# Kernel tuning notes

Hardware: AMD Instinct MI355X
Metric: run time of the kernel (lower is better)

Reference implementation:

```python
import jax, jax.numpy as jnp
import numpy as np

D_MODEL = 1280
NUM_HEADS = 16
GROUPS = 5
D_K = D_MODEL // NUM_HEADS  # 80
B, S = 4, 1024


def setup_inputs() -> dict:
    key = jax.random.key(0)
    ks = jax.random.split(key, 12)
    lim_dk = 1.0 / np.sqrt(D_K)
    lim_dm = 1.0 / np.sqrt(D_MODEL)
    return {
        "src": jax.random.normal(ks[0], (B, S, D_MODEL), jnp.float32),
        "k": jax.random.normal(ks[1], (B, S, D_MODEL), jnp.float32),
        "v": jax.random.normal(ks[2], (B, S, D_MODEL), jnp.float32),
        # per-head Linear(d_k, d_k) stacked: weight [H, d_k(out), d_k(in)], bias [H, d_k]
        "Wq": jax.random.uniform(ks[3], (NUM_HEADS, D_K, D_K), jnp.float32, -lim_dk, lim_dk),
        "bq": jax.random.uniform(ks[4], (NUM_HEADS, D_K), jnp.float32, -lim_dk, lim_dk),
        "Wk": jax.random.uniform(ks[5], (NUM_HEADS, D_K, D_K), jnp.float32, -lim_dk, lim_dk),
        "bk": jax.random.uniform(ks[6], (NUM_HEADS, D_K), jnp.float32, -lim_dk, lim_dk),
        "Wv": jax.random.uniform(ks[7], (NUM_HEADS, D_K, D_K), jnp.float32, -lim_dk, lim_dk),
        "bv": jax.random.uniform(ks[8], (NUM_HEADS, D_K), jnp.float32, -lim_dk, lim_dk),
        # output Linear(d_model, d_model)
        "Wo": jax.random.uniform(ks[9], (D_MODEL, D_MODEL), jnp.float32, -lim_dm, lim_dm),
        "bo": jax.random.uniform(ks[10], (D_MODEL,), jnp.float32, -lim_dm, lim_dm),
    }


def reference(src, k, v, Wq, bq, Wk, bk, Wv, bv, Wo, bo):
    # NOTE: original module ignores k, v args; q/k/v all derived from src.
    b, s, d = src.shape
    cpg = d // GROUPS
    # channel shuffle: [B,S,G,C] -> [B,S,C,G] -> [B,S,D]
    x = src.reshape(b, s, GROUPS, cpg).swapaxes(-1, -2).reshape(b, s, d)
    # split heads: [B, H, S, d_k]
    xh = x.reshape(b, s, NUM_HEADS, D_K).transpose(0, 2, 1, 3)
    # per-head distinct linears, batched over heads (torch Linear: x @ W.T + b)
    q = jnp.einsum("bhsd,hed->bhse", xh, Wq) + bq[None, :, None, :]
    kk = jnp.einsum("bhsd,hed->bhse", xh, Wk) + bk[None, :, None, :]
    vv = jnp.einsum("bhsd,hed->bhse", xh, Wv) + bv[None, :, None, :]
    scores = jnp.einsum("bhqd,bhkd->bhqk", q, kk) / jnp.sqrt(jnp.float32(D_K))
    p = jax.nn.softmax(scores, axis=-1)
    heads = jnp.einsum("bhqk,bhkd->bhqd", p, vv)
    concat = heads.transpose(0, 2, 1, 3).reshape(b, s, d)
    return concat @ Wo.T + bo
```

## Files before the change

kernel.cpp:

```cpp
#include <hip/hip_runtime.h>
#include <hip/hip_bf16.h>

#define D_MODEL 1280
#define NUM_HEADS 16
#define D_K 80
#define DP 96
#define SEQ 1024
#define BATCH 4
#define BH (BATCH*NUM_HEADS)

typedef __hip_bfloat16 bf16;
typedef short short8 __attribute__((ext_vector_type(8)));
typedef short short4v __attribute__((ext_vector_type(4)));
typedef float f32x4 __attribute__((ext_vector_type(4)));

__device__ __forceinline__ float b2f(bf16 x) { return __bfloat162float(x); }
__device__ __forceinline__ bf16 f2b(float x) { return __float2bfloat16(x); }
__device__ __forceinline__ short bbits(float x) {
    union { bf16 b; short s; } u; u.b = __float2bfloat16(x); return u.s;
}

#define MFMA16(a, b, c) __builtin_amdgcn_mfma_f32_16x16x32_bf16(a, b, c, 0, 0, 0)

__global__ __launch_bounds__(256) void cvtw_kernel(
    const float* __restrict__ Wq, const float* __restrict__ Wk,
    const float* __restrict__ Wv, bf16* __restrict__ Wcat)
{
    int idx = blockIdx.x * 256 + threadIdx.x;
    int col = idx % 96;
    int row = (idx / 96) % 240;
    int h   = idx / (96 * 240);
    int mat = row / 80, e = row % 80;
    const float* W = (mat == 0) ? Wq : (mat == 1) ? Wk : Wv;
    float v = (col < 80) ? W[(size_t)(h * 80 + e) * 80 + col] : 0.f;
    Wcat[idx] = f2b(v);
}

__global__ __launch_bounds__(256) void cvt_kernel(
    const float* __restrict__ Wo, bf16* __restrict__ Wb)
{
    int idx = (blockIdx.x * 256 + threadIdx.x) * 4;
    float4 v = *(const float4*)(Wo + idx);
    Wb[idx]     = f2b(v.x);
    Wb[idx + 1] = f2b(v.y);
    Wb[idx + 2] = f2b(v.z);
    Wb[idx + 3] = f2b(v.w);
}

__global__ __launch_bounds__(256) void qkv_kernel(
    const float* __restrict__ src,
    const float* __restrict__ bq, const float* __restrict__ bk,
    const float* __restrict__ bv, const bf16* __restrict__ Wcat,
    bf16* __restrict__ Qb, bf16* __restrict__ Kb, bf16* __restrict__ Vg)
{
    __shared__ bf16 Xs[128 * 104];
    const int h = blockIdx.y;
    const int b = blockIdx.x >> 3;
    const int s0 = (blockIdx.x & 7) * 128;
    const int tid = threadIdx.x;
    const int wave = tid >> 6, lane = tid & 63;
    const int lquad = lane >> 4, lcol = lane & 15;
    const int bh = b * NUM_HEADS + h;

    #pragma unroll
    for (int it = 0; it < 10; it++) {
        int idx = tid + it * 256;
        int i = idx / 20, rem = idx % 20, c = rem >> 2, q4 = rem & 3;
        float4 v = *(const float4*)(src + (size_t)(b * SEQ + s0 + i) * D_MODEL
                                    + c * 256 + h * 16 + q4 * 4);
        bf16* x = Xs + i * 104 + c;
        x[(q4 * 4 + 0) * 5] = f2b(v.x);
        x[(q4 * 4 + 1) * 5] = f2b(v.y);
        x[(q4 * 4 + 2) * 5] = f2b(v.z);
        x[(q4 * 4 + 3) * 5] = f2b(v.w);
    }
    {
        int i = tid >> 1, half = tid & 1;
        *(uint4*)(Xs + i * 104 + 80 + half * 8) = make_uint4(0, 0, 0, 0);
    }
    __syncthreads();

    short8 xf[2][3];
    #pragma unroll
    for (int mt = 0; mt < 2; mt++)
        #pragma unroll
        for (int ks = 0; ks < 3; ks++)
            xf[mt][ks] = *(const short8*)(Xs + (wave*32 + mt*16 + lcol)*104 + ks*32 + lquad*8);

    const bf16* Wh = Wcat + (size_t)h * 240 * 96;
    const float qscale = 1.4426950408889634f * 0.11180339887498949f;

    #pragma unroll
    for (int mat = 0; mat < 2; mat++) {
        const bf16* Wm = Wh + mat * 80 * 96;
        short8 wf[5][3];
        #pragma unroll
        for (int n = 0; n < 5; n++)
            #pragma unroll
            for (int ks = 0; ks < 3; ks++)
                wf[n][ks] = *(const short8*)(Wm + (n*16 + lcol)*96 + ks*32 + lquad*8);

        f32x4 acc[2][5];
        #pragma unroll
        for (int mt = 0; mt < 2; mt++)
            #pragma unroll
            for (int n = 0; n < 5; n++)
                #pragma unroll
                for (int r = 0; r < 4; r++) acc[mt][n][r] = 0.f;

        #pragma unroll
        for (int ks = 0; ks < 3; ks++)
            #pragma unroll
            for (int n = 0; n < 5; n++) {
                acc[0][n] = MFMA16(xf[0][ks], wf[n][ks], acc[0][n]);
                acc[1][n] = MFMA16(xf[1][ks], wf[n][ks], acc[1][n]);
            }

        const float* bias = (mat == 0) ? bq : bk;
        bf16* Out = (mat == 0) ? Qb : Kb;
        const float scale = (mat == 0) ? qscale : 1.f;
        #pragma unroll
        for (int n = 0; n < 5; n++) {
            float bb = bias[h * 80 + n * 16 + lcol];
            #pragma unroll
            for (int mt = 0; mt < 2; mt++)
                #pragma unroll
                for (int r = 0; r < 4; r++) {
                    int srow = s0 + wave*32 + mt*16 + lquad*4 + r;
                    Out[((size_t)bh * SEQ + srow) * DP + n*16 + lcol] =
                        f2b((acc[mt][n][r] + bb) * scale);
                }
        }
    }
    {
        int i = tid >> 1, half = tid & 1;
        size_t row = ((size_t)bh * SEQ + s0 + i) * DP + 80 + half * 8;
        *(uint4*)(Qb + row) = make_uint4(0, 0, 0, 0);
        *(uint4*)(Kb + row) = make_uint4(0, 0, 0, 0);
    }

    {
        const bf16* Wm = Wh + 2 * 80 * 96;
        short8 wf[5][3];
        #pragma unroll
        for (int m = 0; m < 5; m++)
            #pragma unroll
            for (int ks = 0; ks < 3; ks++)
                wf[m][ks] = *(const short8*)(Wm + (m*16 + lcol)*96 + ks*32 + lquad*8);

        f32x4 acc[5][2];
        #pragma unroll
        for (int m = 0; m < 5; m++)
            #pragma unroll
            for (int nt = 0; nt < 2; nt++)
                #pragma unroll
                for (int r = 0; r < 4; r++) acc[m][nt][r] = 0.f;

        #pragma unroll
        for (int ks = 0; ks < 3; ks++)
            #pragma unroll
            for (int m = 0; m < 5; m++) {
                acc[m][0] = MFMA16(wf[m][ks], xf[0][ks], acc[m][0]);
                acc[m][1] = MFMA16(wf[m][ks], xf[1][ks], acc[m][1]);
            }

        #pragma unroll
        for (int m = 0; m < 5; m++) {
            float4 bb4 = *(const float4*)(bv + h * 80 + m * 16 + lquad * 4);
            float bb[4] = {bb4.x, bb4.y, bb4.z, bb4.w};
            #pragma unroll
            for (int nt = 0; nt < 2; nt++)
                #pragma unroll
                for (int r = 0; r < 4; r++) {
                    int e = m*16 + lquad*4 + r;
                    int token = s0 + wave*32 + nt*16 + lcol;
                    Vg[((size_t)bh * D_K + e) * SEQ + token] =
                        f2b(acc[m][nt][r] + bb[r]);
                }
        }
    }
}

__global__ __launch_bounds__(128) void attn_kernel(
    const bf16* __restrict__ Qb, const bf16* __restrict__ Kb,
    const bf16* __restrict__ Vg, bf16* __restrict__ Cc)
{
    __shared__ char smem[38144];
    bf16* Qs = (bf16*)smem;
    bf16* Ks = (bf16*)(smem + 13312);
    bf16* Vt = (bf16*)(smem + 26624);

    const int tid = threadIdx.x;
    const int wave = tid >> 6, lane = tid & 63;
    const int lquad = lane >> 4, lcol = lane & 15;
    const int bh = blockIdx.x;
    const int b = bh >> 4, h = bh & 15;
    const int q0 = blockIdx.y * 64;

    {
        const uint4* qg = (const uint4*)(Qb + ((size_t)bh * SEQ + q0) * DP);
        #pragma unroll
        for (int i = 0; i < 6; i++) {
            int idx = tid + i * 128, r = idx / 12, c = idx % 12;
            *(uint4*)(Qs + r * 104 + c * 8) = qg[idx];
        }
    }
    __syncthreads();

    short8 qf[2][3];
    #pragma unroll
    for (int nt = 0; nt < 2; nt++)
        #pragma unroll
        for (int ks = 0; ks < 3; ks++)
            qf[nt][ks] = *(const short8*)(Qs + (wave*32 + nt*16 + lcol)*104 + ks*32 + lquad*8);

    f32x4 Oacc[2][5];
    #pragma unroll
    for (int mt = 0; mt < 2; mt++)
        #pragma unroll
        for (int ne = 0; ne < 5; ne++)
            #pragma unroll
            for (int r = 0; r < 4; r++) Oacc[mt][ne][r] = 0.f;

    float lsum[2] = {0.f, 0.f};
    bf16* Pw = (bf16*)(smem + wave * 4608);

    for (int kt = 0; kt < 16; kt++) {
        __syncthreads();
        {
            const uint4* kg = (const uint4*)(Kb + ((size_t)bh * SEQ + kt * 64) * DP);
            #pragma unroll
            for (int i = 0; i < 6; i++) {
                int idx = tid + i * 128, r = idx / 12, c = idx % 12;
                *(uint4*)(Ks + r * 104 + c * 8) = kg[idx];
            }
        }
        #pragma unroll
        for (int i = 0; i < 5; i++) {
            int idx = tid + i * 128;
            int e = idx >> 3, c = idx & 7;
            *(uint4*)(Vt + e * 72 + c * 8) =
                *(const uint4*)(Vg + ((size_t)bh * D_K + e) * SEQ + kt * 64 + c * 8);
        }
        __syncthreads();

        f32x4 st[4][2];
        #pragma unroll
        for (int mt = 0; mt < 4; mt++)
            #pragma unroll
            for (int nt = 0; nt < 2; nt++)
                #pragma unroll
                for (int r = 0; r < 4; r++) st[mt][nt][r] = 0.f;

        #pragma unroll
        for (int ks = 0; ks < 3; ks++) {
            #pragma unroll
            for (int mt = 0; mt < 4; mt++) {
                short8 af = *(const short8*)(Ks + (mt*16 + lcol)*104 + ks*32 + lquad*8);
                st[mt][0] = MFMA16(af, qf[0][ks], st[mt][0]);
                st[mt][1] = MFMA16(af, qf[1][ks], st[mt][1]);
            }
        }

        #pragma unroll
        for (int nt = 0; nt < 2; nt++) {
            #pragma unroll
            for (int mt = 0; mt < 4; mt++) {
                short4v pk;
                #pragma unroll
                for (int r = 0; r < 4; r++) {
                    float p = __builtin_amdgcn_exp2f(st[mt][nt][r]);
                    lsum[nt] += p;
                    pk[r] = bbits(p);
                }
                *(short4v*)(Pw + (nt*16 + lcol)*72 + mt*16 + lquad*4) = pk;
            }
        }

        #pragma unroll
        for (int js = 0; js < 2; js++) {
            short8 pf[2];
            #pragma unroll
            for (int mt = 0; mt < 2; mt++)
                pf[mt] = *(const short8*)(Pw + (mt*16 + lcol)*72 + js*32 + lquad*8);
            #pragma unroll
            for (int ne = 0; ne < 5; ne++) {
                short8 vf = *(const short8*)(Vt + (ne*16 + lcol)*72 + js*32 + lquad*8);
                Oacc[0][ne] = MFMA16(pf[0], vf, Oacc[0][ne]);
                Oacc[1][ne] = MFMA16(pf[1], vf, Oacc[1][ne]);
            }
        }
    }

    float inv[2];
    #pragma unroll
    for (int nt = 0; nt < 2; nt++) {
        float s = lsum[nt];
        s += __shfl_xor(s, 16);
        s += __shfl_xor(s, 32);
        inv[nt] = 1.f / s;
    }
    #pragma unroll
    for (int mt = 0; mt < 2; mt++) {
        f32x4 li;
        #pragma unroll
        for (int r = 0; r < 4; r++)
            li[r] = __shfl(inv[mt], (lane & 48) | (lquad*4 + r));
        #pragma unroll
        for (int ne = 0; ne < 5; ne++)
            #pragma unroll
            for (int r = 0; r < 4; r++) {
                int s_row = q0 + wave*32 + mt*16 + lquad*4 + r;
                int e = ne*16 + lcol;
                Cc[(size_t)(b * SEQ + s_row) * D_MODEL + h * D_K + e] =
                    f2b(Oacc[mt][ne][r] * li[r]);
            }
    }
}

__global__ __launch_bounds__(256) void proj_kernel(
    const bf16* __restrict__ Cc, const bf16* __restrict__ Wb,
    const float* __restrict__ bo, float* __restrict__ out)
{
    __shared__ bf16 As[128 * 72];
    __shared__ bf16 Bs[128 * 72];
    const int tid = threadIdx.x;
    const int wave = tid >> 6, lane = tid & 63;
    const int lquad = lane >> 4, lcol = lane & 15;
    const int t0 = blockIdx.x * 128, o0 = blockIdx.y * 128;
    const int mrow = (wave & 1) * 64, ncol = (wave >> 1) * 64;

    f32x4 acc[4][4];
    #pragma unroll
    for (int mt = 0; mt < 4; mt++)
        #pragma unroll
        for (int nt = 0; nt < 4; nt++)
            #pragma unroll
            for (int r = 0; r < 4; r++) acc[mt][nt][r] = 0.f;

    for (int kc = 0; kc < 20; kc++) {
        __syncthreads();
        #pragma unroll
        for (int i = 0; i < 4; i++) {
            int idx = tid + i * 256;
            int r = idx >> 3, c = idx & 7;
            *(uint4*)(As + r * 72 + c * 8) =
                *(const uint4*)(Cc + (size_t)(t0 + r) * D_MODEL + kc * 64 + c * 8);
            *(uint4*)(Bs + r * 72 + c * 8) =
                *(const uint4*)(Wb + (size_t)(o0 + r) * D_MODEL + kc * 64 + c * 8);
        }
        __syncthreads();
        #pragma unroll
        for (int ks = 0; ks < 2; ks++) {
            short8 am[4], bn[4];
            #pragma unroll
            for (int t = 0; t < 4; t++) {
                am[t] = *(const short8*)(As + (mrow + t*16 + lcol)*72 + ks*32 + lquad*8);
                bn[t] = *(const short8*)(Bs + (ncol + t*16 + lcol)*72 + ks*32 + lquad*8);
            }
            #pragma unroll
            for (int mt = 0; mt < 4; mt++)
                #pragma unroll
                for (int nt = 0; nt < 4; nt++)
                    acc[mt][nt] = MFMA16(am[mt], bn[nt], acc[mt][nt]);
        }
    }

    #pragma unroll
    for (int nt = 0; nt < 4; nt++) {
        float bias = bo[o0 + ncol + nt*16 + lcol];
        #pragma unroll
        for (int mt = 0; mt < 4; mt++)
            #pragma unroll
            for (int r = 0; r < 4; r++)
                out[(size_t)(t0 + mrow + mt*16 + lquad*4 + r) * D_MODEL
                    + o0 + ncol + nt*16 + lcol] = acc[mt][nt][r] + bias;
    }
}

extern "C" void kernel_launch(void* const* d_in, const int* in_sizes, int n_in,
                              void* d_out, int out_size, void* d_ws, size_t ws_size,
                              hipStream_t stream) {
    const float* src = (const float*)d_in[0];
    const float* Wq = (const float*)d_in[3];
    const float* bq = (const float*)d_in[4];
    const float* Wk = (const float*)d_in[5];
    const float* bk = (const float*)d_in[6];
    const float* Wv = (const float*)d_in[7];
    const float* bv = (const float*)d_in[8];
    const float* Wo = (const float*)d_in[9];
    const float* bo = (const float*)d_in[10];
    float* out = (float*)d_out;

    char* ws = (char*)d_ws;
    bf16* Qb = (bf16*)(ws);
    bf16* Kb = (bf16*)(ws + (size_t)12582912);
    bf16* Vg = (bf16*)(ws + (size_t)25165824);
    bf16* Cc = (bf16*)(ws + (size_t)35651584);
    bf16* Wcat = (bf16*)(ws + (size_t)35651584);
    bf16* Wb = (bf16*)(ws + (size_t)46137344);

    cvtw_kernel<<<dim3(1440), 256, 0, stream>>>(Wq, Wk, Wv, Wcat);
    cvt_kernel<<<dim3(D_MODEL * D_MODEL / 1024), 256, 0, stream>>>(Wo, Wb);
    qkv_kernel<<<dim3(BATCH * SEQ / 128, NUM_HEADS), 256, 0, stream>>>(
        src, bq, bk, bv, Wcat, Qb, Kb, Vg);
    attn_kernel<<<dim3(BH, SEQ / 64), 128, 0, stream>>>(Qb, Kb, Vg, Cc);
    proj_kernel<<<dim3(SEQ * BATCH / 128, D_MODEL / 128), 256, 0, stream>>>(
        Cc, Wb, bo, out);
}
```

Measured before the change: 197.0 us.

## Double-buffer K tiles, read V directly to registers, merge weight conversion kernels

Reworks the attention kernel to use 256-thread blocks covering 128 queries, keep Q fragments in registers loaded straight from global memory, and double-buffer K tiles in shared memory with register prefetch. This cuts the barriers per iteration from two to one. V fragments are read directly from global into registers instead of being staged through LDS, and s_setprio is raised around the MFMA sections. The two weight-conversion kernels are merged into one launch to remove a launch. The trade-off is more register pressure and uncoalesced per-lane V loads from global memory.

```diff
diff --git a/kernel.cpp b/kernel.cpp
--- a/kernel.cpp
+++ b/kernel.cpp
@@ -22,29 +22,28 @@
 
 #define MFMA16(a, b, c) __builtin_amdgcn_mfma_f32_16x16x32_bf16(a, b, c, 0, 0, 0)
 
-__global__ __launch_bounds__(256) void cvtw_kernel(
+__global__ __launch_bounds__(256) void cvt_all_kernel(
     const float* __restrict__ Wq, const float* __restrict__ Wk,
-    const float* __restrict__ Wv, bf16* __restrict__ Wcat)
-{
-    int idx = blockIdx.x * 256 + threadIdx.x;
-    int col = idx % 96;
-    int row = (idx / 96) % 240;
-    int h   = idx / (96 * 240);
-    int mat = row / 80, e = row % 80;
-    const float* W = (mat == 0) ? Wq : (mat == 1) ? Wk : Wv;
-    float v = (col < 80) ? W[(size_t)(h * 80 + e) * 80 + col] : 0.f;
-    Wcat[idx] = f2b(v);
-}
-
-__global__ __launch_bounds__(256) void cvt_kernel(
+    const float* __restrict__ Wv, bf16* __restrict__ Wcat,
     const float* __restrict__ Wo, bf16* __restrict__ Wb)
 {
-    int idx = (blockIdx.x * 256 + threadIdx.x) * 4;
-    float4 v = *(const float4*)(Wo + idx);
-    Wb[idx]     = f2b(v.x);
-    Wb[idx + 1] = f2b(v.y);
-    Wb[idx + 2] = f2b(v.z);
-    Wb[idx + 3] = f2b(v.w);
+    if (blockIdx.x < 1440) {
+        int idx = blockIdx.x * 256 + threadIdx.x;
+        int col = idx % 96;
+        int row = (idx / 96) % 240;
+        int h   = idx / (96 * 240);
+        int mat = row / 80, e = row % 80;
+        const float* W = (mat == 0) ? Wq : (mat == 1) ? Wk : Wv;
+        float v = (col < 80) ? W[(size_t)(h * 80 + e) * 80 + col] : 0.f;
+        Wcat[idx] = f2b(v);
+    } else {
+        int idx = ((blockIdx.x - 1440) * 256 + threadIdx.x) * 4;
+        float4 v = *(const float4*)(Wo + idx);
+        Wb[idx]     = f2b(v.x);
+        Wb[idx + 1] = f2b(v.y);
+        Wb[idx + 2] = f2b(v.z);
+        Wb[idx + 3] = f2b(v.w);
+    }
 }
 
 __global__ __launch_bounds__(256) void qkv_kernel(
@@ -181,121 +180,143 @@
     }
 }
 
-__global__ __launch_bounds__(128) void attn_kernel(
+__global__ __launch_bounds__(256, 2) void attn_kernel(
     const bf16* __restrict__ Qb, const bf16* __restrict__ Kb,
     const bf16* __restrict__ Vg, bf16* __restrict__ Cc)
 {
-    __shared__ char smem[38144];
-    bf16* Qs = (bf16*)smem;
-    bf16* Ks = (bf16*)(smem + 13312);
-    bf16* Vt = (bf16*)(smem + 26624);
-
+    __shared__ char smem[45056];
     const int tid = threadIdx.x;
     const int wave = tid >> 6, lane = tid & 63;
     const int lquad = lane >> 4, lcol = lane & 15;
     const int bh = blockIdx.x;
     const int b = bh >> 4, h = bh & 15;
-    const int q0 = blockIdx.y * 64;
-
+    const int q0 = blockIdx.y * 128;
+
+    int koff[3];
+    #pragma unroll
+    for (int i = 0; i < 3; i++) {
+        int idx = tid + i * 256;
+        koff[i] = (idx / 12) * 104 + (idx % 12) * 8;
+    }
+
+    short8 qf[2][3];
+    #pragma unroll
+    for (int nt = 0; nt < 2; nt++)
+        #pragma unroll
+        for (int ks = 0; ks < 3; ks++)
+            qf[nt][ks] = *(const short8*)(
+                Qb + ((size_t)bh * SEQ + q0 + wave*32 + nt*16 + lcol) * DP
+                   + ks*32 + lquad*8);
+
+    uint4 kr[3];
     {
-        const uint4* qg = (const uint4*)(Qb + ((size_t)bh * SEQ + q0) * DP);
-        #pragma unroll
-        for (int i = 0; i < 6; i++) {
-            int idx = tid + i * 128, r = idx / 12, c = idx % 12;
-            *(uint4*)(Qs + r * 104 + c * 8) = qg[idx];
-        }
+        const uint4* kg = (const uint4*)(Kb + (size_t)bh * SEQ * DP);
+        #pragma unroll
+        for (int i = 0; i < 3; i++) kr[i] = kg[tid + i * 256];
+    }
+    {
+        bf16* Ks0 = (bf16*)(smem + 18432);
+        #pragma unroll
+        for (int i = 0; i < 3; i++) *(uint4*)(Ks0 + koff[i]) = kr[i];
     }
     __syncthreads();
 
-    short8 qf[2][3];
+    const bf16* Vrow[5];
+    #pragma unroll
+    for (int ne = 0; ne < 5; ne++)
+        Vrow[ne] = Vg + ((size_t)bh * D_K + ne*16 + lcol) * SEQ + lquad*8;
+
+    f32x4 Oacc[2][5];
+    #pragma unroll
+    for (int mt = 0; mt < 2; mt++)
+        #pragma unroll
+        for (int ne = 0; ne < 5; ne++)
+            #pragma unroll
+            for (int r = 0; r < 4; r++) Oacc[mt][ne][r] = 0.f;
+
+    f32x4 lsum4[2];
     #pragma unroll
     for (int nt = 0; nt < 2; nt++)
         #pragma unroll
-        for (int ks = 0; ks < 3; ks++)
-            qf[nt][ks] = *(const short8*)(Qs + (wave*32 + nt*16 + lcol)*104 + ks*32 + lquad*8);
-
-    f32x4 Oacc[2][5];
-    #pragma unroll
-    for (int mt = 0; mt < 2; mt++)
-        #pragma unroll
-        for (int ne = 0; ne < 5; ne++)
-            #pragma unroll
-            for (int r = 0; r < 4; r++) Oacc[mt][ne][r] = 0.f;
-
-    float lsum[2] = {0.f, 0.f};
+        for (int r = 0; r < 4; r++) lsum4[nt][r] = 0.f;
+
     bf16* Pw = (bf16*)(smem + wave * 4608);
+    const f32x4 fzero = {0.f, 0.f, 0.f, 0.f};
 
     for (int kt = 0; kt < 16; kt++) {
-        __syncthreads();
-        {
-            const uint4* kg = (const uint4*)(Kb + ((size_t)bh * SEQ + kt * 64) * DP);
-            #pragma unroll
-            for (int i = 0; i < 6; i++) {
-                int idx = tid + i * 128, r = idx / 12, c = idx % 12;
-                *(uint4*)(Ks + r * 104 + c * 8) = kg[idx];
-            }
-        }
-        #pragma unroll
-        for (int i = 0; i < 5; i++) {
-            int idx = tid + i * 128;
-            int e = idx >> 3, c = idx & 7;
-            *(uint4*)(Vt + e * 72 + c * 8) =
-                *(const uint4*)(Vg + ((size_t)bh * D_K + e) * SEQ + kt * 64 + c * 8);
-        }
-        __syncthreads();
+        const bf16* Ksc = (const bf16*)(smem + 18432 + (kt & 1) * 13312);
+
+        short8 vf[2][5];
+        #pragma unroll
+        for (int js = 0; js < 2; js++)
+            #pragma unroll
+            for (int ne = 0; ne < 5; ne++)
+                vf[js][ne] = *(const short8*)(Vrow[ne] + kt*64 + js*32);
+
+        if (kt < 15) {
+            const uint4* kg = (const uint4*)(
+                Kb + ((size_t)bh * SEQ + (kt + 1) * 64) * DP);
+            #pragma unroll
+            for (int i = 0; i < 3; i++) kr[i] = kg[tid + i * 256];
+        }
 
         f32x4 st[4][2];
-        #pragma unroll
-        for (int mt = 0; mt < 4; mt++)
-            #pragma unroll
-            for (int nt = 0; nt < 2; nt++)
-                #pragma unroll
-                for (int r = 0; r < 4; r++) st[mt][nt][r] = 0.f;
-
-        #pragma unroll
-        for (int ks = 0; ks < 3; ks++) {
+        __builtin_amdgcn_s_setprio(1);
+        #pragma unroll
+        for (int mt = 0; mt < 4; mt++) {
+            short8 af = *(const short8*)(Ksc + (mt*16 + lcol)*104 + lquad*8);
+            st[mt][0] = MFMA16(af, qf[0][0], fzero);
+            st[mt][1] = MFMA16(af, qf[1][0], fzero);
+        }
+        #pragma unroll
+        for (int ks = 1; ks < 3; ks++)
             #pragma unroll
             for (int mt = 0; mt < 4; mt++) {
-                short8 af = *(const short8*)(Ks + (mt*16 + lcol)*104 + ks*32 + lquad*8);
+                short8 af = *(const short8*)(Ksc + (mt*16 + lcol)*104 + ks*32 + lquad*8);
                 st[mt][0] = MFMA16(af, qf[0][ks], st[mt][0]);
                 st[mt][1] = MFMA16(af, qf[1][ks], st[mt][1]);
             }
-        }
-
-        #pragma unroll
-        for (int nt = 0; nt < 2; nt++) {
+        __builtin_amdgcn_s_setprio(0);
+
+        #pragma unroll
+        for (int nt = 0; nt < 2; nt++)
             #pragma unroll
             for (int mt = 0; mt < 4; mt++) {
                 short4v pk;
                 #pragma unroll
                 for (int r = 0; r < 4; r++) {
                     float p = __builtin_amdgcn_exp2f(st[mt][nt][r]);
-                    lsum[nt] += p;
+                    lsum4[nt][r] += p;
                     pk[r] = bbits(p);
                 }
                 *(short4v*)(Pw + (nt*16 + lcol)*72 + mt*16 + lquad*4) = pk;
             }
-        }
-
+
+        __builtin_amdgcn_s_setprio(1);
         #pragma unroll
         for (int js = 0; js < 2; js++) {
-            short8 pf[2];
-            #pragma unroll
-            for (int mt = 0; mt < 2; mt++)
-                pf[mt] = *(const short8*)(Pw + (mt*16 + lcol)*72 + js*32 + lquad*8);
+            short8 pf0 = *(const short8*)(Pw + lcol*72 + js*32 + lquad*8);
+            short8 pf1 = *(const short8*)(Pw + (16 + lcol)*72 + js*32 + lquad*8);
             #pragma unroll
             for (int ne = 0; ne < 5; ne++) {
-                short8 vf = *(const short8*)(Vt + (ne*16 + lcol)*72 + js*32 + lquad*8);
-                Oacc[0][ne] = MFMA16(pf[0], vf, Oacc[0][ne]);
-                Oacc[1][ne] = MFMA16(pf[1], vf, Oacc[1][ne]);
-            }
+                Oacc[0][ne] = MFMA16(pf0, vf[js][ne], Oacc[0][ne]);
+                Oacc[1][ne] = MFMA16(pf1, vf[js][ne], Oacc[1][ne]);
+            }
+        }
+        __builtin_amdgcn_s_setprio(0);
+
+        if (kt < 15) {
+            bf16* Ksn = (bf16*)(smem + 18432 + ((kt + 1) & 1) * 13312);
+            #pragma unroll
+            for (int i = 0; i < 3; i++) *(uint4*)(Ksn + koff[i]) = kr[i];
+            __syncthreads();
         }
     }
 
     float inv[2];
     #pragma unroll
     for (int nt = 0; nt < 2; nt++) {
-        float s = lsum[nt];
+        float s = (lsum4[nt][0] + lsum4[nt][1]) + (lsum4[nt][2] + lsum4[nt][3]);
         s += __shfl_xor(s, 16);
         s += __shfl_xor(s, 32);
         inv[nt] = 1.f / s;
@@ -400,11 +421,10 @@
     bf16* Wcat = (bf16*)(ws + (size_t)35651584);
     bf16* Wb = (bf16*)(ws + (size_t)46137344);
 
-    cvtw_kernel<<<dim3(1440), 256, 0, stream>>>(Wq, Wk, Wv, Wcat);
-    cvt_kernel<<<dim3(D_MODEL * D_MODEL / 1024), 256, 0, stream>>>(Wo, Wb);
+    cvt_all_kernel<<<dim3(3040), 256, 0, stream>>>(Wq, Wk, Wv, Wcat, Wo, Wb);
     qkv_kernel<<<dim3(BATCH * SEQ / 128, NUM_HEADS), 256, 0, stream>>>(
         src, bq, bk, bv, Wcat, Qb, Kb, Vg);
-    attn_kernel<<<dim3(BH, SEQ / 64), 128, 0, stream>>>(Qb, Kb, Vg, Cc);
+    attn_kernel<<<dim3(BH, SEQ / 128), 256, 0, stream>>>(Qb, Kb, Vg, Cc);
     proj_kernel<<<dim3(SEQ * BATCH / 128, D_MODEL / 128), 256, 0, stream>>>(
         Cc, Wb, bo, out);
 }
```

Measured after the change: 204.6 us. 3.9% more time.
